# Optimization experiments

Hardware: AMD Instinct MI355X
Metric: run time of the kernel (lower is better)

The kernel has to match this reference:

```python
import jax, jax.numpy as jnp
import numpy as np

B, S, H, NH, MLP = 4, 2048, 768, 12, 3072
HD = H // NH  # 64
EPS = 1e-6


def layernorm(x, w, b):
    m = jnp.mean(x, axis=-1, keepdims=True)
    v = jnp.mean(jnp.square(x - m), axis=-1, keepdims=True)
    return (x - m) * jax.lax.rsqrt(v + EPS) * w + b


def setup_inputs() -> dict:
    key = jax.random.key(0)
    ks = jax.random.split(key, 16)
    s = 0.02
    return {
        "x": jax.random.normal(ks[0], (B, S, H), dtype=jnp.float32),
        "ln1_w": jnp.ones((H,), jnp.float32),
        "ln1_b": jnp.zeros((H,), jnp.float32),
        "wq": jax.random.normal(ks[1], (H, H), jnp.float32) * s,
        "bq": jnp.zeros((H,), jnp.float32),
        "wk": jax.random.normal(ks[2], (H, H), jnp.float32) * s,
        "bk": jnp.zeros((H,), jnp.float32),
        "wv": jax.random.normal(ks[3], (H, H), jnp.float32) * s,
        "bv": jnp.zeros((H,), jnp.float32),
        "wo": jax.random.normal(ks[4], (H, H), jnp.float32) * s,
        "bo": jnp.zeros((H,), jnp.float32),
        "ln2_w": jnp.ones((H,), jnp.float32),
        "ln2_b": jnp.zeros((H,), jnp.float32),
        "w1": jax.random.normal(ks[5], (H, MLP), jnp.float32) * s,
        "b1": jnp.zeros((MLP,), jnp.float32),
        "w2": jax.random.normal(ks[6], (MLP, H), jnp.float32) * s,
        "b2": jnp.zeros((H,), jnp.float32),
    }


def reference(x, ln1_w, ln1_b, wq, bq, wk, bk, wv, bv, wo, bo,
              ln2_w, ln2_b, w1, b1, w2, b2):
    # --- attention sub-block (pre-norm) ---
    h = x
    xn = layernorm(x, ln1_w, ln1_b)
    q = (xn @ wq + bq).reshape(B, S, NH, HD)
    k = (xn @ wk + bk).reshape(B, S, NH, HD)
    v = (xn @ wv + bv).reshape(B, S, NH, HD)
    scores = jnp.einsum('bqhd,bkhd->bhqk', q, k) / jnp.sqrt(jnp.float32(HD))
    probs = jax.nn.softmax(scores, axis=-1)  # [B,NH,S,S] materialized, as in source
    ctx = jnp.einsum('bhqk,bkhd->bqhd', probs, v).reshape(B, S, H)
    x = ctx @ wo + bo + h
    # --- MLP sub-block (pre-norm) ---
    h = x
    xn = layernorm(x, ln2_w, ln2_b)
    y = jax.nn.gelu(xn @ w1 + b1, approximate=False)  # nn.GELU default = exact erf
    x = y @ w2 + b2 + h
    return x
```

## Files before the change

kernel.cpp:

```cpp
#include <hip/hip_runtime.h>
#include <hip/hip_bf16.h>

#define B_ 4
#define S_ 2048
#define H_ 768
#define NH_ 12
#define HD_ 64
#define MLP_ 3072
#define M_ (B_*S_)

typedef float f32x4 __attribute__((ext_vector_type(4)));
typedef short bf16x8 __attribute__((ext_vector_type(8)));

__device__ __forceinline__ short f2bf(float f) {
  union { float f; unsigned u; } x; x.f = f;
  unsigned r = (x.u + 0x7fffu + ((x.u >> 16) & 1u)) >> 16;
  return (short)(unsigned short)r;
}

__device__ __forceinline__ float exp2g(float x) {
  float r; asm("v_exp_f32 %0, %1" : "=v"(r) : "v"(x)); return r;
}
__device__ __forceinline__ float rcpg(float x) {
  float r; asm("v_rcp_f32 %0, %1" : "=v"(r) : "v"(x)); return r;
}
__device__ __forceinline__ unsigned cvtpk(float a, float b) {
  unsigned r; asm("v_cvt_pk_bf16_f32 %0, %1, %2" : "=v"(r) : "v"(a), "v"(b)); return r;
}

typedef __attribute__((address_space(1))) const void gvoid;
typedef __attribute__((address_space(3))) void lvoid;
__device__ __forceinline__ void async16(const void* g, void* l) {
  __builtin_amdgcn_global_load_lds((gvoid*)g, (lvoid*)l, 16, 0, 0);
}

__device__ __forceinline__ int xcd_swz(int h, int nwg) {
  const int q = nwg >> 3, r = nwg & 7;
  const int xc = h & 7, i = h >> 3;
  return (xc < r ? xc * (q + 1) : r * (q + 1) + (xc - r) * q) + i;
}

__global__ __launch_bounds__(256)
void tcast(const float* __restrict__ in, short* __restrict__ out, int K, int N) {
  __shared__ float tile[32][33];
  const int n0 = blockIdx.x * 32, k0 = blockIdx.y * 32;
  const int tx = threadIdx.x, ty = threadIdx.y;
#pragma unroll
  for (int i = 0; i < 4; ++i)
    tile[ty * 4 + i][tx] = in[(size_t)(k0 + ty * 4 + i) * N + n0 + tx];
  __syncthreads();
#pragma unroll
  for (int i = 0; i < 4; ++i)
    out[(size_t)(n0 + ty * 4 + i) * K + k0 + tx] = f2bf(tile[tx][ty * 4 + i]);
}

__global__ __launch_bounds__(256)
void tcast4(const float* __restrict__ i0, const float* __restrict__ i1,
            const float* __restrict__ i2, const float* __restrict__ i3,
            short* __restrict__ o0, short* __restrict__ o1,
            short* __restrict__ o2, short* __restrict__ o3) {
  __shared__ float tile[32][33];
  const int z = blockIdx.z;
  const float* in = (z == 0) ? i0 : (z == 1) ? i1 : (z == 2) ? i2 : i3;
  short* out = (z == 0) ? o0 : (z == 1) ? o1 : (z == 2) ? o2 : o3;
  const int n0 = blockIdx.x * 32, k0 = blockIdx.y * 32;
  const int tx = threadIdx.x, ty = threadIdx.y;
#pragma unroll
  for (int i = 0; i < 4; ++i)
    tile[ty * 4 + i][tx] = in[(size_t)(k0 + ty * 4 + i) * 768 + n0 + tx];
  __syncthreads();
#pragma unroll
  for (int i = 0; i < 4; ++i)
    out[(size_t)(n0 + ty * 4 + i) * 768 + k0 + tx] = f2bf(tile[tx][ty * 4 + i]);
}

__device__ __forceinline__ float block_sum256(float v) {
  __shared__ float red[4];
#pragma unroll
  for (int o = 32; o > 0; o >>= 1) v += __shfl_down(v, o);
  if ((threadIdx.x & 63) == 0) red[threadIdx.x >> 6] = v;
  __syncthreads();
  v = red[0] + red[1] + red[2] + red[3];
  __syncthreads();
  return v;
}

__global__ __launch_bounds__(256)
void ln_fwd(const float* __restrict__ xin, const float* __restrict__ g,
            const float* __restrict__ bt, short* __restrict__ o) {
  const int row = blockIdx.x, t = threadIdx.x;
  const float* xr = xin + (size_t)row * H_;
  const float v0 = xr[t], v1 = xr[t + 256], v2 = xr[t + 512];
  const float mean = block_sum256(v0 + v1 + v2) * (1.0f / H_);
  const float d0 = v0 - mean, d1 = v1 - mean, d2 = v2 - mean;
  const float var = block_sum256(d0 * d0 + d1 * d1 + d2 * d2) * (1.0f / H_);
  const float rstd = rsqrtf(var + 1e-6f);
  short* orow = o + (size_t)row * H_;
  orow[t]       = f2bf(d0 * rstd * g[t] + bt[t]);
  orow[t + 256] = f2bf(d1 * rstd * g[t + 256] + bt[t + 256]);
  orow[t + 512] = f2bf(d2 * rstd * g[t + 512] + bt[t + 512]);
}

#define QSCALE 0.18033688011112042f
template<int MODE>
__global__ __launch_bounds__(256)
void gemm_bt(const short* __restrict__ A, const short* __restrict__ Bw,
             int K, int N,
             const float* __restrict__ b0, const float* __restrict__ b1,
             const float* __restrict__ b2,
             const float* __restrict__ resid,
             float* __restrict__ outf, short* __restrict__ outh,
             short* __restrict__ oq, short* __restrict__ ok2, short* __restrict__ ov) {
  __shared__ short As[2][128 * 64];
  __shared__ short Bs[2][64 * 64];
  const int tid = threadIdx.x;
  const int wv = tid >> 6, lane = tid & 63;
  const int lo = lane & 15, hi = lane >> 4;
  const int wr = wv >> 1, wc = wv & 1;

  const int GX = gridDim.x;
  const int logical = xcd_swz(blockIdx.y * GX + blockIdx.x, GX * gridDim.y);
  const int bn = logical % GX, bm = logical / GX;

  const short* Ab = A + (size_t)bm * 128 * K;
  const short* Bb = Bw + (size_t)bn * 64 * K;
  const int srow = lane >> 3;
  const int scol = ((lane & 7) ^ srow) * 8;

  auto stage = [&](int buf, int kt) {
#pragma unroll
    for (int c = 0; c < 4; ++c) {
      const int rb = wv * 32 + c * 8;
      async16(Ab + (size_t)(rb + srow) * K + kt + scol, &As[buf][rb * 64]);
    }
#pragma unroll
    for (int c = 0; c < 2; ++c) {
      const int rb = wv * 16 + c * 8;
      async16(Bb + (size_t)(rb + srow) * K + kt + scol, &Bs[buf][rb * 64]);
    }
  };

  f32x4 acc[4][2] = {};
  stage(0, 0);
  const int nIt = K >> 6;
  for (int it = 0; it < nIt; ++it) {
    __syncthreads();
    if (it + 1 < nIt) stage((it + 1) & 1, (it + 1) << 6);
    const short* as = As[it & 1];
    const short* bs = Bs[it & 1];
#pragma unroll
    for (int ks = 0; ks < 2; ++ks) {
      const int rc = (((ks * 4 + hi) ^ (lo & 7)) * 8);
      bf16x8 af[4], bfr[2];
#pragma unroll
      for (int m = 0; m < 4; ++m)
        af[m] = *(const bf16x8*)&as[(wr * 64 + m * 16 + lo) * 64 + rc];
#pragma unroll
      for (int n = 0; n < 2; ++n)
        bfr[n] = *(const bf16x8*)&bs[(wc * 32 + n * 16 + lo) * 64 + rc];
#pragma unroll
      for (int m = 0; m < 4; ++m)
#pragma unroll
        for (int n = 0; n < 2; ++n)
          acc[m][n] = __builtin_amdgcn_mfma_f32_16x16x32_bf16(af[m], bfr[n], acc[m][n], 0, 0, 0);
    }
  }
  const int colBase = bn * 64 + wc * 32;
  const int rowBase = bm * 128 + wr * 64;
#pragma unroll
  for (int m = 0; m < 4; ++m) {
#pragma unroll
    for (int n = 0; n < 2; ++n) {
#pragma unroll
      for (int r = 0; r < 4; ++r) {
        const int row = rowBase + m * 16 + hi * 4 + r;
        const int col = colBase + n * 16 + lo;
        float val = acc[m][n][r];
        if (MODE == 0) {
          const int which = col / H_;
          const int nn = col - which * H_;
          val += (which == 0 ? b0 : which == 1 ? b1 : b2)[nn];
          if (which == 0) val *= QSCALE;
          const int h = nn >> 6, d = nn & 63;
          const int bI = row >> 11, s = row & (S_ - 1);
          const short bv16 = f2bf(val);
          if (which == 2) {
            const int sl = s & 63;
            const int pc = ((sl >> 4) & 1) * 32 + ((sl >> 2) & 3) * 8
                         + ((sl >> 5) & 1) * 4 + (sl & 3);
            ov[(((size_t)bI * NH_ + h) * HD_ + d) * S_ + (s & ~63) + pc] = bv16;
          } else {
            short* dst = (which == 0 ? oq : ok2);
            dst[(((size_t)bI * NH_ + h) * S_ + s) * HD_ + d] = bv16;
          }
        } else if (MODE == 1) {
          val += b0[col] + resid[(size_t)row * N + col];
          outf[(size_t)row * N + col] = val;
        } else {
          val += b0[col];
          const float u = val * (0.7978845608f + 0.0356774081f * val * val);
          const float e = exp2g(-2.885390082f * u);
          val = val * rcpg(1.0f + e);
          outh[(size_t)row * N + col] = f2bf(val);
        }
      }
    }
  }
}

__global__ __launch_bounds__(256)
void attn_fwd(const short* __restrict__ qbuf, const short* __restrict__ kbuf,
              const short* __restrict__ vbuf, short* __restrict__ ctx) {
  __shared__ short Ks[8 * 512];
  __shared__ short Vt[8 * 512];
  const int tid = threadIdx.x;
  const int wv = tid >> 6, lane = tid & 63;
  const int lo = lane & 15, hi = lane >> 4;
  const int logical = xcd_swz(blockIdx.y * 32 + blockIdx.x, 32 * 48);
  const int qt = logical & 31, bh = logical >> 5;
  const int bI = bh / NH_, h = bh - bI * NH_;
  const size_t baseBH = (size_t)bh * S_ * HD_;
  const int q0 = qt * 64 + wv * 16;

  bf16x8 qf[2];
#pragma unroll
  for (int ks = 0; ks < 2; ++ks)
    qf[ks] = *(const bf16x8*)&qbuf[baseBH + (size_t)(q0 + lo) * HD_ + ks * 32 + hi * 8];

  f32x4 accc[4] = {};
  float mrow = 0.0f, lsum = 0.0f;

  const short* ksrc = kbuf + baseBH + (size_t)(wv * 16 + lo) * HD_ + hi * 8;
  const short* vsrc = vbuf + baseBH + (size_t)(wv * 16 + lo) * S_ + hi * 8;
  short* kdst0 = &Ks[wv * 1024 + lane * 8];
  short* kdst1 = kdst0 + 512;
  short* vdst0 = &Vt[wv * 1024 + lane * 8];
  short* vdst1 = vdst0 + 512;

  bf16x8 kreg0, kreg1, vreg0, vreg1;
  kreg0 = *(const bf16x8*)(ksrc);
  kreg1 = *(const bf16x8*)(ksrc + 32);
  vreg0 = *(const bf16x8*)(vsrc);
  vreg1 = *(const bf16x8*)(vsrc + 32);

  for (int kt = 0; kt < S_; kt += 64) {
    __syncthreads();
    *(bf16x8*)kdst0 = kreg0;
    *(bf16x8*)kdst1 = kreg1;
    *(bf16x8*)vdst0 = vreg0;
    *(bf16x8*)vdst1 = vreg1;
    if (kt + 64 < S_) {
      const short* kp = ksrc + (size_t)(kt + 64) * HD_;
      kreg0 = *(const bf16x8*)(kp);
      kreg1 = *(const bf16x8*)(kp + 32);
      const short* vp = vsrc + kt + 64;
      vreg0 = *(const bf16x8*)(vp);
      vreg1 = *(const bf16x8*)(vp + 32);
    }
    __syncthreads();
    f32x4 sc[4];
    __builtin_amdgcn_s_setprio(1);
#pragma unroll
    for (int nk = 0; nk < 4; ++nk) {
      f32x4 z = {0.f, 0.f, 0.f, 0.f};
#pragma unroll
      for (int ks = 0; ks < 2; ++ks) {
        bf16x8 kf = *(const bf16x8*)&Ks[(nk * 2 + ks) * 512 + lane * 8];
        z = __builtin_amdgcn_mfma_f32_16x16x32_bf16(kf, qf[ks], z, 0, 0, 0);
      }
      sc[nk] = z;
    }
    __builtin_amdgcn_s_setprio(0);
    const float m0 = fmaxf(fmaxf(sc[0][0], sc[0][1]), fmaxf(sc[0][2], sc[0][3]));
    const float m1 = fmaxf(fmaxf(sc[1][0], sc[1][1]), fmaxf(sc[1][2], sc[1][3]));
    const float m2 = fmaxf(fmaxf(sc[2][0], sc[2][1]), fmaxf(sc[2][2], sc[2][3]));
    const float m3 = fmaxf(fmaxf(sc[3][0], sc[3][1]), fmaxf(sc[3][2], sc[3][3]));
    float mx = fmaxf(fmaxf(m0, m1), fmaxf(m2, m3));
    mx = fmaxf(mx, __shfl_xor(mx, 16));
    mx = fmaxf(mx, __shfl_xor(mx, 32));
#pragma unroll
    for (int nk = 0; nk < 4; ++nk)
#pragma unroll
      for (int r = 0; r < 4; ++r)
        sc[nk][r] = exp2g(sc[nk][r] - mrow);
    if (!__all(mx <= mrow + 8.0f)) {
      const float mnew = fmaxf(mrow, mx);
      const float alpha = exp2g(mrow - mnew);
      lsum *= alpha;
#pragma unroll
      for (int nk = 0; nk < 4; ++nk)
#pragma unroll
        for (int r = 0; r < 4; ++r) sc[nk][r] *= alpha;
#pragma unroll
      for (int r = 0; r < 4; ++r) {
        const float aA = __shfl(alpha, hi * 4 + r);
#pragma unroll
        for (int nd = 0; nd < 4; ++nd) accc[nd][r] *= aA;
      }
      mrow = mnew;
    }
    {
      const float t0 = (sc[0][0] + sc[0][1]) + (sc[0][2] + sc[0][3]);
      const float t1 = (sc[1][0] + sc[1][1]) + (sc[1][2] + sc[1][3]);
      const float t2 = (sc[2][0] + sc[2][1]) + (sc[2][2] + sc[2][3]);
      const float t3 = (sc[3][0] + sc[3][1]) + (sc[3][2] + sc[3][3]);
      lsum += (t0 + t1) + (t2 + t3);
    }
    union PU { unsigned u[4]; bf16x8 v; } pa0, pa1;
    pa0.u[0] = cvtpk(sc[0][0], sc[0][1]); pa0.u[1] = cvtpk(sc[0][2], sc[0][3]);
    pa0.u[2] = cvtpk(sc[2][0], sc[2][1]); pa0.u[3] = cvtpk(sc[2][2], sc[2][3]);
    pa1.u[0] = cvtpk(sc[1][0], sc[1][1]); pa1.u[1] = cvtpk(sc[1][2], sc[1][3]);
    pa1.u[2] = cvtpk(sc[3][0], sc[3][1]); pa1.u[3] = cvtpk(sc[3][2], sc[3][3]);
    __builtin_amdgcn_s_setprio(1);
#pragma unroll
    for (int nd = 0; nd < 4; ++nd) {
      bf16x8 vf0 = *(const bf16x8*)&Vt[(nd * 2 + 0) * 512 + lane * 8];
      accc[nd] = __builtin_amdgcn_mfma_f32_16x16x32_bf16(pa0.v, vf0, accc[nd], 0, 0, 0);
      bf16x8 vf1 = *(const bf16x8*)&Vt[(nd * 2 + 1) * 512 + lane * 8];
      accc[nd] = __builtin_amdgcn_mfma_f32_16x16x32_bf16(pa1.v, vf1, accc[nd], 0, 0, 0);
    }
    __builtin_amdgcn_s_setprio(0);
  }
  lsum += __shfl_xor(lsum, 16);
  lsum += __shfl_xor(lsum, 32);
#pragma unroll
  for (int r = 0; r < 4; ++r) {
    const float inv = 1.0f / __shfl(lsum, hi * 4 + r);
    const int srow = q0 + hi * 4 + r;
    const size_t rowoff = ((size_t)bI * S_ + srow) * H_ + h * HD_;
#pragma unroll
    for (int nd = 0; nd < 4; ++nd)
      ctx[rowoff + nd * 16 + lo] = f2bf(accc[nd][r] * inv);
  }
}

extern "C" void kernel_launch(void* const* d_in, const int* in_sizes, int n_in,
                              void* d_out, int out_size, void* d_ws, size_t ws_size,
                              hipStream_t stream) {
  const float* x    = (const float*)d_in[0];
  const float* ln1w = (const float*)d_in[1];
  const float* ln1b = (const float*)d_in[2];
  const float* wq   = (const float*)d_in[3];
  const float* bq   = (const float*)d_in[4];
  const float* wk   = (const float*)d_in[5];
  const float* bk   = (const float*)d_in[6];
  const float* wvp  = (const float*)d_in[7];
  const float* bv   = (const float*)d_in[8];
  const float* wo   = (const float*)d_in[9];
  const float* bo   = (const float*)d_in[10];
  const float* ln2w = (const float*)d_in[11];
  const float* ln2b = (const float*)d_in[12];
  const float* w1   = (const float*)d_in[13];
  const float* b1   = (const float*)d_in[14];
  const float* w2   = (const float*)d_in[15];
  const float* b2   = (const float*)d_in[16];
  float* out = (float*)d_out;

  short* ws = (short*)d_ws;
  short* wqkvT = ws;
  short* woT   = wqkvT + (size_t)2304 * 768;
  short* w1T   = woT + (size_t)768 * 768;
  short* w2T   = w1T + (size_t)3072 * 768;
  short* xn    = w2T + (size_t)768 * 3072;
  short* qb    = xn + (size_t)M_ * H_;
  short* kb    = qb + (size_t)M_ * H_;
  short* vb    = kb + (size_t)M_ * H_;
  short* ctx   = vb + (size_t)M_ * H_;
  short* yb    = qb;
  float* x1    = (float*)(ctx + (size_t)M_ * H_);

  dim3 tb(32, 8);
  tcast4<<<dim3(24, 24, 4), tb, 0, stream>>>(wq, wk, wvp, wo,
      wqkvT, wqkvT + (size_t)768 * 768, wqkvT + (size_t)2 * 768 * 768, woT);
  tcast<<<dim3(96, 24), tb, 0, stream>>>(w1, w1T, 768, 3072);
  tcast<<<dim3(24, 96), tb, 0, stream>>>(w2, w2T, 3072, 768);

  ln_fwd<<<M_, 256, 0, stream>>>(x, ln1w, ln1b, xn);

  gemm_bt<0><<<dim3(36, 64), 256, 0, stream>>>(xn, wqkvT, 768, 2304,
      bq, bk, bv, nullptr, nullptr, nullptr, qb, kb, vb);

  attn_fwd<<<dim3(32, 48), 256, 0, stream>>>(qb, kb, vb, ctx);

  gemm_bt<1><<<dim3(12, 64), 256, 0, stream>>>(ctx, woT, 768, 768,
      bo, nullptr, nullptr, x, x1, nullptr, nullptr, nullptr, nullptr);

  ln_fwd<<<M_, 256, 0, stream>>>(x1, ln2w, ln2b, xn);

  gemm_bt<2><<<dim3(48, 64), 256, 0, stream>>>(xn, w1T, 768, 3072,
      b1, nullptr, nullptr, nullptr, nullptr, yb, nullptr, nullptr, nullptr);

  gemm_bt<1><<<dim3(12, 64), 256, 0, stream>>>(yb, w2T, 3072, 768,
      b2, nullptr, nullptr, x1, out, nullptr, nullptr, nullptr, nullptr);
}
```

Before: 315.4 us.

## Double-buffer attention K/V tiles and compute row sums via MFMA

Splits the K and V shared-memory tiles into two buffers so the next tile is written while the current one is consumed, which cuts the two barriers per iteration down to one. The softmax denominator is now accumulated with an extra MFMA against a ones vector, which takes the per-iteration VALU adds and end-of-loop shuffles off the critical path. The max cross-lane shuffles also move inside the rare rescale branch. In exchange it doubles LDS use, adds two MFMAs per tile, and prefetches with a clamped redundant load on the last iterations.

```diff
diff --git a/kernel.cpp b/kernel.cpp
--- a/kernel.cpp
+++ b/kernel.cpp
@@ -211,8 +211,8 @@
 __global__ __launch_bounds__(256)
 void attn_fwd(const short* __restrict__ qbuf, const short* __restrict__ kbuf,
               const short* __restrict__ vbuf, short* __restrict__ ctx) {
-  __shared__ short Ks[8 * 512];
-  __shared__ short Vt[8 * 512];
+  __shared__ short Ks[2][8 * 512];
+  __shared__ short Vt[2][8 * 512];
   const int tid = threadIdx.x;
   const int wv = tid >> 6, lane = tid & 63;
   const int lo = lane & 15, hi = lane >> 4;
@@ -228,65 +228,76 @@
     qf[ks] = *(const bf16x8*)&qbuf[baseBH + (size_t)(q0 + lo) * HD_ + ks * 32 + hi * 8];
 
   f32x4 accc[4] = {};
-  float mrow = 0.0f, lsum = 0.0f;
+  f32x4 accS = {};
+  float mrow = 0.0f;
+
+  const short oo = (lo == 0) ? (short)0x3F80 : (short)0;
+  const bf16x8 onesf = {oo, oo, oo, oo, oo, oo, oo, oo};
 
   const short* ksrc = kbuf + baseBH + (size_t)(wv * 16 + lo) * HD_ + hi * 8;
   const short* vsrc = vbuf + baseBH + (size_t)(wv * 16 + lo) * S_ + hi * 8;
-  short* kdst0 = &Ks[wv * 1024 + lane * 8];
-  short* kdst1 = kdst0 + 512;
-  short* vdst0 = &Vt[wv * 1024 + lane * 8];
-  short* vdst1 = vdst0 + 512;
+  const int dst0 = wv * 1024 + lane * 8;
 
   bf16x8 kreg0, kreg1, vreg0, vreg1;
   kreg0 = *(const bf16x8*)(ksrc);
   kreg1 = *(const bf16x8*)(ksrc + 32);
   vreg0 = *(const bf16x8*)(vsrc);
   vreg1 = *(const bf16x8*)(vsrc + 32);
-
-  for (int kt = 0; kt < S_; kt += 64) {
-    __syncthreads();
-    *(bf16x8*)kdst0 = kreg0;
-    *(bf16x8*)kdst1 = kreg1;
-    *(bf16x8*)vdst0 = vreg0;
-    *(bf16x8*)vdst1 = vreg1;
-    if (kt + 64 < S_) {
-      const short* kp = ksrc + (size_t)(kt + 64) * HD_;
+  *(bf16x8*)&Ks[0][dst0] = kreg0;
+  *(bf16x8*)&Ks[0][dst0 + 512] = kreg1;
+  *(bf16x8*)&Vt[0][dst0] = vreg0;
+  *(bf16x8*)&Vt[0][dst0 + 512] = vreg1;
+  kreg0 = *(const bf16x8*)(ksrc + (size_t)64 * HD_);
+  kreg1 = *(const bf16x8*)(ksrc + (size_t)64 * HD_ + 32);
+  vreg0 = *(const bf16x8*)(vsrc + 64);
+  vreg1 = *(const bf16x8*)(vsrc + 64 + 32);
+  __syncthreads();
+
+  for (int t = 0; t < S_ / 64; ++t) {
+    const int cur = t & 1, nxt = cur ^ 1;
+    const short* ks = Ks[cur];
+    const short* vt = Vt[cur];
+    f32x4 sc[4];
+    __builtin_amdgcn_s_setprio(1);
+#pragma unroll
+    for (int nk = 0; nk < 4; ++nk) {
+      f32x4 z = {0.f, 0.f, 0.f, 0.f};
+#pragma unroll
+      for (int k2 = 0; k2 < 2; ++k2) {
+        bf16x8 kf = *(const bf16x8*)&ks[(nk * 2 + k2) * 512 + lane * 8];
+        z = __builtin_amdgcn_mfma_f32_16x16x32_bf16(kf, qf[k2], z, 0, 0, 0);
+      }
+      sc[nk] = z;
+    }
+    __builtin_amdgcn_s_setprio(0);
+    *(bf16x8*)&Ks[nxt][dst0] = kreg0;
+    *(bf16x8*)&Ks[nxt][dst0 + 512] = kreg1;
+    *(bf16x8*)&Vt[nxt][dst0] = vreg0;
+    *(bf16x8*)&Vt[nxt][dst0 + 512] = vreg1;
+    {
+      const int tn = (t + 2 < S_ / 64) ? t + 2 : S_ / 64 - 1;
+      const short* kp = ksrc + (size_t)tn * 64 * HD_;
       kreg0 = *(const bf16x8*)(kp);
       kreg1 = *(const bf16x8*)(kp + 32);
-      const short* vp = vsrc + kt + 64;
+      const short* vp = vsrc + tn * 64;
       vreg0 = *(const bf16x8*)(vp);
       vreg1 = *(const bf16x8*)(vp + 32);
     }
-    __syncthreads();
-    f32x4 sc[4];
-    __builtin_amdgcn_s_setprio(1);
-#pragma unroll
-    for (int nk = 0; nk < 4; ++nk) {
-      f32x4 z = {0.f, 0.f, 0.f, 0.f};
-#pragma unroll
-      for (int ks = 0; ks < 2; ++ks) {
-        bf16x8 kf = *(const bf16x8*)&Ks[(nk * 2 + ks) * 512 + lane * 8];
-        z = __builtin_amdgcn_mfma_f32_16x16x32_bf16(kf, qf[ks], z, 0, 0, 0);
-      }
-      sc[nk] = z;
-    }
-    __builtin_amdgcn_s_setprio(0);
     const float m0 = fmaxf(fmaxf(sc[0][0], sc[0][1]), fmaxf(sc[0][2], sc[0][3]));
     const float m1 = fmaxf(fmaxf(sc[1][0], sc[1][1]), fmaxf(sc[1][2], sc[1][3]));
     const float m2 = fmaxf(fmaxf(sc[2][0], sc[2][1]), fmaxf(sc[2][2], sc[2][3]));
     const float m3 = fmaxf(fmaxf(sc[3][0], sc[3][1]), fmaxf(sc[3][2], sc[3][3]));
     float mx = fmaxf(fmaxf(m0, m1), fmaxf(m2, m3));
-    mx = fmaxf(mx, __shfl_xor(mx, 16));
-    mx = fmaxf(mx, __shfl_xor(mx, 32));
 #pragma unroll
     for (int nk = 0; nk < 4; ++nk)
 #pragma unroll
       for (int r = 0; r < 4; ++r)
         sc[nk][r] = exp2g(sc[nk][r] - mrow);
     if (!__all(mx <= mrow + 8.0f)) {
+      mx = fmaxf(mx, __shfl_xor(mx, 16));
+      mx = fmaxf(mx, __shfl_xor(mx, 32));
       const float mnew = fmaxf(mrow, mx);
       const float alpha = exp2g(mrow - mnew);
-      lsum *= alpha;
 #pragma unroll
       for (int nk = 0; nk < 4; ++nk)
 #pragma unroll
@@ -294,17 +305,11 @@
 #pragma unroll
       for (int r = 0; r < 4; ++r) {
         const float aA = __shfl(alpha, hi * 4 + r);
+        accS[r] *= aA;
 #pragma unroll
         for (int nd = 0; nd < 4; ++nd) accc[nd][r] *= aA;
       }
       mrow = mnew;
-    }
-    {
-      const float t0 = (sc[0][0] + sc[0][1]) + (sc[0][2] + sc[0][3]);
-      const float t1 = (sc[1][0] + sc[1][1]) + (sc[1][2] + sc[1][3]);
-      const float t2 = (sc[2][0] + sc[2][1]) + (sc[2][2] + sc[2][3]);
-      const float t3 = (sc[3][0] + sc[3][1]) + (sc[3][2] + sc[3][3]);
-      lsum += (t0 + t1) + (t2 + t3);
     }
     union PU { unsigned u[4]; bf16x8 v; } pa0, pa1;
     pa0.u[0] = cvtpk(sc[0][0], sc[0][1]); pa0.u[1] = cvtpk(sc[0][2], sc[0][3]);
@@ -312,20 +317,21 @@
     pa1.u[0] = cvtpk(sc[1][0], sc[1][1]); pa1.u[1] = cvtpk(sc[1][2], sc[1][3]);
     pa1.u[2] = cvtpk(sc[3][0], sc[3][1]); pa1.u[3] = cvtpk(sc[3][2], sc[3][3]);
     __builtin_amdgcn_s_setprio(1);
+    accS = __builtin_amdgcn_mfma_f32_16x16x32_bf16(pa0.v, onesf, accS, 0, 0, 0);
+    accS = __builtin_amdgcn_mfma_f32_16x16x32_bf16(pa1.v, onesf, accS, 0, 0, 0);
 #pragma unroll
     for (int nd = 0; nd < 4; ++nd) {
-      bf16x8 vf0 = *(const bf16x8*)&Vt[(nd * 2 + 0) * 512 + lane * 8];
+      bf16x8 vf0 = *(const bf16x8*)&vt[(nd * 2 + 0) * 512 + lane * 8];
       accc[nd] = __builtin_amdgcn_mfma_f32_16x16x32_bf16(pa0.v, vf0, accc[nd], 0, 0, 0);
-      bf16x8 vf1 = *(const bf16x8*)&Vt[(nd * 2 + 1) * 512 + lane * 8];
+      bf16x8 vf1 = *(const bf16x8*)&vt[(nd * 2 + 1) * 512 + lane * 8];
       accc[nd] = __builtin_amdgcn_mfma_f32_16x16x32_bf16(pa1.v, vf1, accc[nd], 0, 0, 0);
     }
     __builtin_amdgcn_s_setprio(0);
+    __syncthreads();
   }
-  lsum += __shfl_xor(lsum, 16);
-  lsum += __shfl_xor(lsum, 32);
 #pragma unroll
   for (int r = 0; r < 4; ++r) {
-    const float inv = 1.0f / __shfl(lsum, hi * 4 + r);
+    const float inv = 1.0f / __shfl(accS[r], hi << 4);
     const int srow = q0 + hi * 4 + r;
     const size_t rowoff = ((size_t)bI * S_ + srow) * H_ + h * HD_;
 #pragma unroll
```

Result: no change. 316.9 us (+0.5%).
